# Kernel tuning notes

Hardware: AMD Instinct MI355X
Metric: run time of the kernel (lower is better)

Reference implementation:

```python
import jax, jax.numpy as jnp
import numpy as np
import math

B, N, F, H, T = 2, 1024, 8, 64, 16
E_R, E_C, EA = 8192, 32768, 4
NF = N * F


def _pos_enc(t_steps, h):
    pe = np.zeros((t_steps, h), dtype=np.float32)
    pos = np.arange(t_steps, dtype=np.float32)[:, None]
    div = np.exp(np.arange(0, h, 2, dtype=np.float32) * -(math.log(10000.0) / h))
    pe[:, 0::2] = np.sin(pos * div)
    pe[:, 1::2] = np.cos(pos * div)
    return jnp.asarray(pe)


def _ln(x, g, b, eps=1e-5):
    m = x.mean(-1, keepdims=True)
    v = jnp.var(x, axis=-1, keepdims=True)
    return (x - m) / jnp.sqrt(v + eps) * g + b


def _lrelu(x):
    return jnp.where(x >= 0, x, 0.01 * x)


def setup_inputs() -> dict:
    key = jax.random.key(0)
    ks = jax.random.split(key, 40)
    s = 0.05
    inp = {
        'x_global': jax.random.normal(ks[0], (B, N, H, T), jnp.float32),
        'per_feature_x': jax.random.normal(ks[1], (B, N, F, H, T), jnp.float32),
        'river_edge_attr': jax.random.uniform(ks[2], (E_R, EA), jnp.float32),
        'causal_edge_weight': jax.random.uniform(ks[3], (E_C,), jnp.float32),
        'W_tc': jax.random.normal(ks[4], (H, H, 3), jnp.float32) * s,
        'b_tc': jnp.zeros((H,), jnp.float32),
        'r_lin_W': jax.random.normal(ks[5], (H, H), jnp.float32) * s,
        'r_lin_b': jnp.zeros((H,), jnp.float32),
        'r_upd_W': jax.random.normal(ks[6], (2 * H, H), jnp.float32) * s,
        'r_upd_b': jnp.zeros((H,), jnp.float32),
        'r_edge_W': jax.random.normal(ks[7], (EA, 1), jnp.float32) * s,
        'r_edge_b': jnp.zeros((1,), jnp.float32),
        'r_gate': jnp.ones((1,), jnp.float32) * 0.3,
        'c_lin_W': jax.random.normal(ks[8], (H, H), jnp.float32) * s,
        'c_lin_b': jnp.zeros((H,), jnp.float32),
        'c_upd_W': jax.random.normal(ks[9], (2 * H, H), jnp.float32) * s,
        'c_upd_b': jnp.zeros((H,), jnp.float32),
        'c_gate': jnp.ones((1,), jnp.float32) * 0.3,
        'sf_W': jax.random.normal(ks[10], (2 * H, H), jnp.float32) * s,
        'sf_b': jnp.zeros((H,), jnp.float32),
        'femb': jax.random.normal(ks[11], (F, H), jnp.float32) * 0.02,
        'pfn_g': jnp.ones((H,), jnp.float32),
        'pfn_b': jnp.zeros((H,), jnp.float32),
        'f1_W': jax.random.normal(ks[12], (2 * H, H), jnp.float32) * s,
        'f1_b': jnp.zeros((H,), jnp.float32),
        'fln_g': jnp.ones((H,), jnp.float32),
        'fln_b': jnp.zeros((H,), jnp.float32),
        'f2_W': jax.random.normal(ks[13], (H, H), jnp.float32) * s,
        'f2_b': jnp.zeros((H,), jnp.float32),
        'river_edge_index': jax.random.randint(ks[14], (2, E_R), 0, N, jnp.int64),
        'causal_edge_index': jax.random.randint(ks[15], (2, E_C), 0, NF, jnp.int64),
    }
    return inp


def reference(x_global, per_feature_x, river_edge_attr, causal_edge_weight,
              W_tc, b_tc, r_lin_W, r_lin_b, r_upd_W, r_upd_b, r_edge_W, r_edge_b, r_gate,
              c_lin_W, c_lin_b, c_upd_W, c_upd_b, c_gate, sf_W, sf_b, femb,
              pfn_g, pfn_b, f1_W, f1_b, fln_g, fln_b, f2_W, f2_b,
              river_edge_index, causal_edge_index):
    b_, n_, h_, t_ = x_global.shape
    f_ = per_feature_x.shape[2]
    nf = n_ * f_

    # ---- river graph conv (vectorized over B,T) ----
    x_bt = jnp.transpose(x_global, (0, 3, 1, 2))  # [B,T,N,H]
    ew = (river_edge_attr @ r_edge_W + r_edge_b)[:, 0]  # edge_encoder -> [E_r]
    mw_r = jnp.clip(jax.nn.sigmoid(r_gate) * ew, 0.0, 1.0)
    src_r, tgt_r = river_edge_index[0], river_edge_index[1]
    lx = x_bt @ r_lin_W + r_lin_b
    msg_r = lx[:, :, src_r, :] * mw_r[None, None, :, None]  # [B,T,E_r,H]
    agg_r = jnp.zeros_like(x_bt).at[:, :, tgt_r, :].add(msg_r)
    river_upd = _lrelu(jnp.concatenate([agg_r, x_bt], -1) @ r_upd_W + r_upd_b)

    # ---- causal graph conv on (basin, feature) nodes ----
    pf_bt = jnp.transpose(per_feature_x, (0, 4, 1, 2, 3))  # [B,T,N,F,H]
    nodes = (pf_bt + femb[None, None, None]).reshape(b_, t_, nf, h_)
    mw_c = jnp.clip(jax.nn.sigmoid(c_gate) * causal_edge_weight, 0.0, 1.0)
    src_c, tgt_c = causal_edge_index[0], causal_edge_index[1]
    clx = nodes @ c_lin_W + c_lin_b
    msg_c = clx[:, :, src_c, :] * mw_c[None, None, :, None]  # [B,T,E_c,H]
    agg_c = jnp.zeros_like(nodes).at[:, :, tgt_c, :].add(msg_c)
    cupd = _lrelu(jnp.concatenate([agg_c, nodes], -1) @ c_upd_W + c_upd_b)
    cupd = cupd.reshape(b_, t_, n_, f_, h_)

    # per-feature layernorm over H, then to [B,N,F,H,T]
    pf_out = _ln(cupd, pfn_g, pfn_b)
    pf_out = jnp.transpose(pf_out, (0, 2, 3, 4, 1))

    causal_pooled = cupd.mean(axis=3)  # [B,T,N,H]
    x_spatial = jax.nn.silu(jnp.concatenate([river_upd, causal_pooled], -1) @ sf_W + sf_b)

    # ---- temporal conv with sin/cos positional encoding ----
    pe = _pos_enc(t_, h_)
    xt = jnp.transpose(x_global, (0, 1, 3, 2)) + pe[None, None]  # [B,N,T,H]
    x_nch = jnp.transpose(xt.reshape(b_ * n_, t_, h_), (0, 2, 1))  # [BN,H,T]
    y = jax.lax.conv_general_dilated(x_nch, W_tc, (1,), [(1, 1)],
                                     dimension_numbers=('NCH', 'OIH', 'NCH'))
    y = y + b_tc[None, :, None]
    x_temporal = jnp.transpose(y, (0, 2, 1)).reshape(b_, n_, t_, h_)

    # ---- fusion ----
    x_sp_bnth = jnp.transpose(x_spatial, (0, 2, 1, 3))  # [B,N,T,H]
    fz = jnp.concatenate([x_temporal, x_sp_bnth], -1) @ f1_W + f1_b
    fz = jax.nn.silu(_ln(fz, fln_g, fln_b))
    fz = fz @ f2_W + f2_b
    x_out = jnp.transpose(fz, (0, 1, 3, 2))  # [B,N,H,T]
    return (x_out, pf_out)
```

## Files before the change

kernel.cpp:

```cpp
#include <hip/hip_runtime.h>
#include <cstddef>

#define BB 2
#define NN 1024
#define FF 8
#define HH 64
#define TT 16
#define ER 8192
#define EC 32768
#define EA 4
#define NFD 8192
#define BTT 32
#define LDA 68

__device__ __forceinline__ void tile_gemm(const float* At, const float* Wt,
                                          float4 acc[4], int r0, int c0) {
#pragma unroll 16
  for (int k = 0; k < 64; ++k) {
    int rsw = r0 ^ (((k >> 4) & 3) << 2);
    float4 a = *(const float4*)(At + k * LDA + rsw);
    float4 b = *(const float4*)(Wt + k * LDA + c0);
    acc[0].x = fmaf(a.x, b.x, acc[0].x); acc[0].y = fmaf(a.x, b.y, acc[0].y);
    acc[0].z = fmaf(a.x, b.z, acc[0].z); acc[0].w = fmaf(a.x, b.w, acc[0].w);
    acc[1].x = fmaf(a.y, b.x, acc[1].x); acc[1].y = fmaf(a.y, b.y, acc[1].y);
    acc[1].z = fmaf(a.y, b.z, acc[1].z); acc[1].w = fmaf(a.y, b.w, acc[1].w);
    acc[2].x = fmaf(a.z, b.x, acc[2].x); acc[2].y = fmaf(a.z, b.y, acc[2].y);
    acc[2].z = fmaf(a.z, b.z, acc[2].z); acc[2].w = fmaf(a.z, b.w, acc[2].w);
    acc[3].x = fmaf(a.w, b.x, acc[3].x); acc[3].y = fmaf(a.w, b.y, acc[3].y);
    acc[3].z = fmaf(a.w, b.z, acc[3].z); acc[3].w = fmaf(a.w, b.w, acc[3].w);
  }
}

__device__ __forceinline__ void stage_W(float* Wt, const float* __restrict__ W, int tid) {
#pragma unroll
  for (int q = 0; q < 4; ++q) {
    int i = tid + q * 256;
    int k = i >> 4, c4 = (i & 15) << 2;
    *(float4*)(Wt + k * LDA + c4) = *(const float4*)(W + k * 64 + c4);
  }
}

__device__ __forceinline__ void stage_AT(float* At, const float* __restrict__ src, int tid) {
  int row = tid >> 2, kc = (tid & 3) << 4;
  int rsw = row ^ ((tid & 3) << 2);
  if (src) {
#pragma unroll
    for (int q = 0; q < 4; ++q) {
      float4 v = *(const float4*)(src + kc + q * 4);
      int k = kc + q * 4;
      At[(k + 0) * LDA + rsw] = v.x;
      At[(k + 1) * LDA + rsw] = v.y;
      At[(k + 2) * LDA + rsw] = v.z;
      At[(k + 3) * LDA + rsw] = v.w;
    }
  } else {
#pragma unroll
    for (int q = 0; q < 16; ++q) At[(kc + q) * LDA + rsw] = 0.f;
  }
}

#define FMA4(P, V) \
  P.x = fmaf(w, V.x, P.x); P.y = fmaf(w, V.y, P.y); \
  P.z = fmaf(w, V.z, P.z); P.w = fmaf(w, V.w, P.w);

__device__ __forceinline__ void stage_gather(float* At, float* s_sh,
                                             const float* __restrict__ slice, int rowbase,
                                             const int2* __restrict__ eg,
                                             const int* __restrict__ off, int tid) {
  int row = tid >> 2, kc = (tid & 3) << 4;
  int rsw = row ^ ((tid & 3) << 2);
  float4 p0 = make_float4(0.f, 0.f, 0.f, 0.f), p1 = p0, p2 = p0, p3 = p0;
  float s = 0.f;
  int node = rowbase + row;
  int e0 = off[node], e1 = off[node + 1];
  int j = e0;
  for (; j + 2 <= e1; j += 2) {
    int2 ea = eg[j], eb = eg[j + 1];
    float wa = __int_as_float(ea.y), wb = __int_as_float(eb.y);
    const float4* spa = (const float4*)(slice + (size_t)ea.x * 64 + kc);
    const float4* spb = (const float4*)(slice + (size_t)eb.x * 64 + kc);
    float4 a0 = spa[0], a1 = spa[1], a2 = spa[2], a3 = spa[3];
    float4 b0 = spb[0], b1 = spb[1], b2 = spb[2], b3 = spb[3];
    { float w = wa; FMA4(p0, a0); FMA4(p1, a1); FMA4(p2, a2); FMA4(p3, a3); }
    { float w = wb; FMA4(p0, b0); FMA4(p1, b1); FMA4(p2, b2); FMA4(p3, b3); }
    s += wa + wb;
  }
  if (j < e1) {
    int2 ea = eg[j];
    float w = __int_as_float(ea.y);
    const float4* spa = (const float4*)(slice + (size_t)ea.x * 64 + kc);
    float4 a0 = spa[0], a1 = spa[1], a2 = spa[2], a3 = spa[3];
    FMA4(p0, a0); FMA4(p1, a1); FMA4(p2, a2); FMA4(p3, a3);
    s += w;
  }
  At[(kc + 0) * LDA + rsw] = p0.x;  At[(kc + 1) * LDA + rsw] = p0.y;
  At[(kc + 2) * LDA + rsw] = p0.z;  At[(kc + 3) * LDA + rsw] = p0.w;
  At[(kc + 4) * LDA + rsw] = p1.x;  At[(kc + 5) * LDA + rsw] = p1.y;
  At[(kc + 6) * LDA + rsw] = p1.z;  At[(kc + 7) * LDA + rsw] = p1.w;
  At[(kc + 8) * LDA + rsw] = p2.x;  At[(kc + 9) * LDA + rsw] = p2.y;
  At[(kc + 10) * LDA + rsw] = p2.z; At[(kc + 11) * LDA + rsw] = p2.w;
  At[(kc + 12) * LDA + rsw] = p3.x; At[(kc + 13) * LDA + rsw] = p3.y;
  At[(kc + 14) * LDA + rsw] = p3.z; At[(kc + 15) * LDA + rsw] = p3.w;
  if ((tid & 3) == 0) s_sh[row] = s;
}

template <bool POOL>
__global__ __launch_bounds__(256, 4) void k_gnn(const float* __restrict__ base,
    const int* __restrict__ off, const int2* __restrict__ eg,
    const float* __restrict__ Wf, const float* __restrict__ Wbot,
    const float* __restrict__ vv, const float* __restrict__ bb,
    float* __restrict__ out, float* __restrict__ pooled,
    int ngShift, int rowsSlice) {
  __shared__ float At[64 * LDA];
  __shared__ float Wt[64 * LDA];
  __shared__ float s_sh[64];
  int tid = threadIdx.x;
  int bid = blockIdx.x;
  int xcd = bid & 7;
  int slot = bid >> 3;
  int ng = slot & ((1 << ngShift) - 1);
  int bt = xcd + 8 * (slot >> ngShift);
  const float* slice = base + (size_t)bt * rowsSlice * 64;
  int rowbase = ng * 64;
  float4 z4 = make_float4(0.f, 0.f, 0.f, 0.f);
  float4 acc[4] = {z4, z4, z4, z4};
  int r0 = (tid >> 4) << 2, c0 = (tid & 15) << 2;

  stage_W(Wt, Wf, tid);
  stage_gather(At, s_sh, slice, rowbase, eg, off, tid);
  __syncthreads();
  tile_gemm(At, Wt, acc, r0, c0);
  __syncthreads();

  stage_W(Wt, Wbot, tid);
  stage_AT(At, slice + (size_t)(rowbase + (tid >> 2)) * 64, tid);
  __syncthreads();
  tile_gemm(At, Wt, acc, r0, c0);

  float4 v4 = *(const float4*)(vv + c0);
  float4 b4 = *(const float4*)(bb + c0);
  float4 zz[4];
#pragma unroll
  for (int i = 0; i < 4; ++i) {
    int row = r0 + i;
    float sv = s_sh[row];
    float4 z;
    z.x = acc[i].x + sv * v4.x + b4.x;
    z.y = acc[i].y + sv * v4.y + b4.y;
    z.z = acc[i].z + sv * v4.z + b4.z;
    z.w = acc[i].w + sv * v4.w + b4.w;
    z.x = z.x >= 0.f ? z.x : 0.01f * z.x;
    z.y = z.y >= 0.f ? z.y : 0.01f * z.y;
    z.z = z.z >= 0.f ? z.z : 0.01f * z.z;
    z.w = z.w >= 0.f ? z.w : 0.01f * z.w;
    zz[i] = z;
    *(float4*)(out + ((size_t)bt * rowsSlice + rowbase + row) * 64 + c0) = z;
  }

  if (POOL) {
    float4 ps;
    ps.x = zz[0].x + zz[1].x + zz[2].x + zz[3].x;
    ps.y = zz[0].y + zz[1].y + zz[2].y + zz[3].y;
    ps.z = zz[0].z + zz[1].z + zz[2].z + zz[3].z;
    ps.w = zz[0].w + zz[1].w + zz[2].w + zz[3].w;
    ps.x += __shfl_xor(ps.x, 16);
    ps.y += __shfl_xor(ps.y, 16);
    ps.z += __shfl_xor(ps.z, 16);
    ps.w += __shfl_xor(ps.w, 16);
    if (((tid >> 4) & 1) == 0) {
      int nd = r0 >> 3;
      float4 o;
      o.x = ps.x * 0.125f; o.y = ps.y * 0.125f;
      o.z = ps.z * 0.125f; o.w = ps.w * 0.125f;
      *(float4*)(pooled + ((size_t)bt * NN + (rowbase >> 3) + nd) * 64 + c0) = o;
    }
  }
}

__global__ __launch_bounds__(256, 4) void k_sf2(const float* __restrict__ river_upd,
    const float* __restrict__ pooled, const float* __restrict__ sf_W,
    const float* __restrict__ sf_b, float* __restrict__ x_spatial) {
  __shared__ float At[64 * LDA];
  __shared__ float Wt[64 * LDA];
  int tid = threadIdx.x;
  int rowbase = blockIdx.x * 64;
  float4 z4 = make_float4(0.f, 0.f, 0.f, 0.f);
  float4 acc[4] = {z4, z4, z4, z4};
  int r0 = (tid >> 4) << 2, c0 = (tid & 15) << 2;

  stage_W(Wt, sf_W, tid);
  stage_AT(At, river_upd + (size_t)(rowbase + (tid >> 2)) * 64, tid);
  __syncthreads();
  tile_gemm(At, Wt, acc, r0, c0);
  __syncthreads();

  stage_W(Wt, sf_W + 4096, tid);
  stage_AT(At, pooled + (size_t)(rowbase + (tid >> 2)) * 64, tid);
  __syncthreads();
  tile_gemm(At, Wt, acc, r0, c0);

  float4 b4 = *(const float4*)(sf_b + c0);
#pragma unroll
  for (int i = 0; i < 4; ++i) {
    float4 z;
    z.x = acc[i].x + b4.x; z.y = acc[i].y + b4.y;
    z.z = acc[i].z + b4.z; z.w = acc[i].w + b4.w;
    z.x = z.x / (1.f + expf(-z.x)); z.y = z.y / (1.f + expf(-z.y));
    z.z = z.z / (1.f + expf(-z.z)); z.w = z.w / (1.f + expf(-z.w));
    *(float4*)(x_spatial + (size_t)(rowbase + r0 + i) * 64 + c0) = z;
  }
}

__global__ __launch_bounds__(256, 4) void k_fuse2(const float* __restrict__ xt,
    const float* __restrict__ xsp, const float* __restrict__ Wg,
    const float* __restrict__ cvec, const float* __restrict__ f1W,
    const float* __restrict__ flng, const float* __restrict__ flnb,
    const float* __restrict__ f2W, const float* __restrict__ f2b,
    float* __restrict__ x_out) {
  __shared__ float At[64 * LDA];
  __shared__ float Wt[64 * LDA];
  int tid = threadIdx.x;
  int bn0 = blockIdx.x * 4;
  int srow = tid >> 2;
  int bnl = srow >> 4, t = srow & 15;
  int bn = bn0 + bnl;
  float4 z4 = make_float4(0.f, 0.f, 0.f, 0.f);
  float4 acc[4] = {z4, z4, z4, z4};
  int r0 = (tid >> 4) << 2, c0 = (tid & 15) << 2;

#pragma unroll
  for (int kt = 0; kt < 3; ++kt) {
    int t2 = t + kt - 1;
    const float* src = (t2 >= 0 && t2 < TT) ? xt + ((size_t)bn * TT + t2) * 64 : nullptr;
    stage_W(Wt, Wg + kt * 4096, tid);
    stage_AT(At, src, tid);
    __syncthreads();
    tile_gemm(At, Wt, acc, r0, c0);
    __syncthreads();
  }
  {
    int b = bn >> 10, n = bn & 1023;
    const float* src = xsp + ((size_t)(b * TT + t) * NN + n) * 64;
    stage_W(Wt, f1W + 4096, tid);
    stage_AT(At, src, tid);
    __syncthreads();
    tile_gemm(At, Wt, acc, r0, c0);
    __syncthreads();
  }

  float4 cv = *(const float4*)(cvec + c0);
  float4 g4 = *(const float4*)(flng + c0);
  float4 lb4 = *(const float4*)(flnb + c0);
  float4 zz[4];
#pragma unroll
  for (int i = 0; i < 4; ++i) {
    zz[i].x = acc[i].x + cv.x; zz[i].y = acc[i].y + cv.y;
    zz[i].z = acc[i].z + cv.z; zz[i].w = acc[i].w + cv.w;
    float ps = zz[i].x + zz[i].y + zz[i].z + zz[i].w;
    float pq = zz[i].x * zz[i].x + zz[i].y * zz[i].y + zz[i].z * zz[i].z + zz[i].w * zz[i].w;
    ps += __shfl_xor(ps, 1); pq += __shfl_xor(pq, 1);
    ps += __shfl_xor(ps, 2); pq += __shfl_xor(pq, 2);
    ps += __shfl_xor(ps, 4); pq += __shfl_xor(pq, 4);
    ps += __shfl_xor(ps, 8); pq += __shfl_xor(pq, 8);
    float m = ps * (1.f / 64.f);
    float var = pq * (1.f / 64.f) - m * m;
    float inv = rsqrtf(var + 1e-5f);
    float4 w;
    w.x = (zz[i].x - m) * inv * g4.x + lb4.x;
    w.y = (zz[i].y - m) * inv * g4.y + lb4.y;
    w.z = (zz[i].z - m) * inv * g4.z + lb4.z;
    w.w = (zz[i].w - m) * inv * g4.w + lb4.w;
    zz[i].x = w.x / (1.f + expf(-w.x));
    zz[i].y = w.y / (1.f + expf(-w.y));
    zz[i].z = w.z / (1.f + expf(-w.z));
    zz[i].w = w.w / (1.f + expf(-w.w));
  }
  {
    int xsw = ((c0 >> 4) & 3) << 2;
#pragma unroll
    for (int i = 0; i < 4; ++i) {
      int rr = (r0 + i) ^ xsw;
      At[(c0 + 0) * LDA + rr] = zz[i].x;
      At[(c0 + 1) * LDA + rr] = zz[i].y;
      At[(c0 + 2) * LDA + rr] = zz[i].z;
      At[(c0 + 3) * LDA + rr] = zz[i].w;
    }
  }
  stage_W(Wt, f2W, tid);
  __syncthreads();
  float4 acc2[4] = {z4, z4, z4, z4};
  tile_gemm(At, Wt, acc2, r0, c0);
  __syncthreads();
  float4 f2b4 = *(const float4*)(f2b + c0);
#pragma unroll
  for (int i = 0; i < 4; ++i) {
    float4 o;
    o.x = acc2[i].x + f2b4.x; o.y = acc2[i].y + f2b4.y;
    o.z = acc2[i].z + f2b4.z; o.w = acc2[i].w + f2b4.w;
    *(float4*)(Wt + (r0 + i) * LDA + c0) = o;
  }
  __syncthreads();
#pragma unroll
  for (int q = 0; q < 4; ++q) {
    int idx = tid + q * 256;
    int fo = idx * 4;
    int bnl2 = fo >> 10, rem = fo & 1023;
    int c = rem >> 4, tt = rem & 15;
    float4 o;
    o.x = Wt[(bnl2 * 16 + tt + 0) * LDA + c];
    o.y = Wt[(bnl2 * 16 + tt + 1) * LDA + c];
    o.z = Wt[(bnl2 * 16 + tt + 2) * LDA + c];
    o.w = Wt[(bnl2 * 16 + tt + 3) * LDA + c];
    *(float4*)(x_out + (size_t)(bn0 + bnl2) * 1024 + rem) = o;
  }
}

__global__ void k_prep_edges(const float* __restrict__ attr, const float* __restrict__ cw,
                             const float* __restrict__ reW, const float* __restrict__ reB,
                             const float* __restrict__ rgate, const float* __restrict__ cgate,
                             float* __restrict__ mw_r, float* __restrict__ mw_c,
                             int* __restrict__ rcnt, int* __restrict__ ccnt) {
  int i = blockIdx.x * 256 + threadIdx.x;
  if (i < EC) {
    float g = 1.f / (1.f + expf(-cgate[0]));
    mw_c[i] = fminf(fmaxf(g * cw[i], 0.f), 1.f);
  }
  if (i < ER) {
    float ew = reB[0];
#pragma unroll
    for (int a = 0; a < EA; ++a) ew += attr[i * EA + a] * reW[a];
    float g = 1.f / (1.f + expf(-rgate[0]));
    mw_r[i] = fminf(fmaxf(g * ew, 0.f), 1.f);
  }
  if (i < NN) rcnt[i] = 0;
  if (i < NFD) ccnt[i] = 0;
}

__global__ void k_prep_w(const float* __restrict__ r_lin_W, const float* __restrict__ r_upd_W,
                         const float* __restrict__ r_lin_b,
                         const float* __restrict__ c_lin_W, const float* __restrict__ c_upd_W,
                         const float* __restrict__ c_lin_b,
                         const float* __restrict__ W_tc, const float* __restrict__ b_tc,
                         const float* __restrict__ f1_W, const float* __restrict__ f1_b,
                         float* __restrict__ Wfr, float* __restrict__ v_r,
                         float* __restrict__ Wfc, float* __restrict__ v_c,
                         float* __restrict__ Wg, float* __restrict__ cvec) {
  int tid = threadIdx.x;
  if (blockIdx.x == 0) {
    for (int idx = tid; idx < 4096; idx += 256) {
      int k = idx >> 6, j = idx & 63;
      float s = 0.f;
      for (int m = 0; m < 64; ++m) s += r_lin_W[k * 64 + m] * r_upd_W[m * 64 + j];
      Wfr[idx] = s;
    }
    if (tid < 64) {
      float s = 0.f;
      for (int m = 0; m < 64; ++m) s += r_lin_b[m] * r_upd_W[m * 64 + tid];
      v_r[tid] = s;
    }
  } else if (blockIdx.x == 1) {
    for (int idx = tid; idx < 4096; idx += 256) {
      int k = idx >> 6, j = idx & 63;
      float s = 0.f;
      for (int m = 0; m < 64; ++m) s += c_lin_W[k * 64 + m] * c_upd_W[m * 64 + j];
      Wfc[idx] = s;
    }
    if (tid < 64) {
      float s = 0.f;
      for (int m = 0; m < 64; ++m) s += c_lin_b[m] * c_upd_W[m * 64 + tid];
      v_c[tid] = s;
    }
  } else {
    for (int idx = tid; idx < 12288; idx += 256) {
      int r = idx >> 6, c = idx & 63;
      int kk = r >> 6, i = r & 63;
      float s = 0.f;
      for (int o = 0; o < 64; ++o) s += W_tc[o * 192 + i * 3 + kk] * f1_W[o * 64 + c];
      Wg[idx] = s;
    }
    if (tid < 64) {
      float s = f1_b[tid];
      for (int o = 0; o < 64; ++o) s += b_tc[o] * f1_W[o * 64 + tid];
      cvec[tid] = s;
    }
  }
}

__global__ void k_count(const int* __restrict__ ridx, const int* __restrict__ cidx,
                        int* __restrict__ rcnt, int* __restrict__ ccnt) {
  int e = blockIdx.x * 256 + threadIdx.x;
  if (e < ER) atomicAdd(&rcnt[ridx[ER + e]], 1);
  if (e < EC) atomicAdd(&ccnt[cidx[EC + e]], 1);
}

template <int ITEMS>
__device__ __forceinline__ void scan_impl(const int* __restrict__ cnt, int n,
                                          int* __restrict__ off, int* __restrict__ cur,
                                          int* sh) {
  int tid = threadIdx.x;
  int local[ITEMS];
  int s = 0;
  int base = tid * ITEMS;
#pragma unroll
  for (int j = 0; j < ITEMS; ++j) { local[j] = cnt[base + j]; s += local[j]; }
  sh[tid] = s;
  __syncthreads();
  for (int d = 1; d < 1024; d <<= 1) {
    int v = (tid >= d) ? sh[tid - d] : 0;
    __syncthreads();
    sh[tid] += v;
    __syncthreads();
  }
  int excl = tid ? sh[tid - 1] : 0;
#pragma unroll
  for (int j = 0; j < ITEMS; ++j) { off[base + j] = excl; cur[base + j] = excl; excl += local[j]; }
  if (tid == 1023) off[n] = excl;
}

__global__ __launch_bounds__(1024) void k_scan(const int* __restrict__ rcnt, int* __restrict__ roff,
                                               int* __restrict__ rcur,
                                               const int* __restrict__ ccnt, int* __restrict__ coff,
                                               int* __restrict__ ccur) {
  __shared__ int sh[1024];
  if (blockIdx.x == 0) scan_impl<1>(rcnt, NN, roff, rcur, sh);
  else                 scan_impl<8>(ccnt, NFD, coff, ccur, sh);
}

__global__ void k_fill(const int* __restrict__ ridx, const int* __restrict__ cidx,
                       const float* __restrict__ mw_r, const float* __restrict__ mw_c,
                       int* __restrict__ rcur, int* __restrict__ ccur,
                       int2* __restrict__ rpk, int2* __restrict__ cpk) {
  int e = blockIdx.x * 256 + threadIdx.x;
  if (e < ER) {
    int t = ridx[ER + e]; int p = atomicAdd(&rcur[t], 1);
    rpk[p] = make_int2(ridx[e], __float_as_int(mw_r[e]));
  }
  if (e < EC) {
    int t = cidx[EC + e]; int p = atomicAdd(&ccur[t], 1);
    cpk[p] = make_int2(cidx[e], __float_as_int(mw_c[e]));
  }
}

__global__ void k_xpose(const float* __restrict__ xg, float* __restrict__ x_bt,
                        float* __restrict__ xt) {
  __shared__ float lds[64][17];
  int bn = blockIdx.x;
  int b = bn >> 10, n = bn & 1023;
  int tid = threadIdx.x;
  const float* src = xg + (size_t)bn * (HH * TT);
  for (int i = tid; i < 1024; i += 256) lds[i >> 4][i & 15] = src[i];
  __syncthreads();
  for (int i = tid; i < 1024; i += 256) {
    int t = i >> 6, h = i & 63;
    float v = lds[h][t];
    float div = expf(-(float)(h & ~1) * (9.210340371976184f / 64.f));
    float arg = (float)t * div;
    float pe = (h & 1) ? cosf(arg) : sinf(arg);
    xt[(size_t)bn * 1024 + i] = v + pe;
    x_bt[(((size_t)b * TT + t) * NN + n) * HH + h] = v;
  }
}

__global__ void k_nodes(const float* __restrict__ pfx, const float* __restrict__ femb,
                        float* __restrict__ nodes) {
  __shared__ float lds[64][17];
  int bnf = blockIdx.x;
  int f = bnf & 7;
  int n = (bnf >> 3) & 1023;
  int b = bnf >> 13;
  int tid = threadIdx.x;
  const float* src = pfx + (size_t)bnf * (HH * TT);
  for (int i = tid; i < 1024; i += 256) lds[i >> 4][i & 15] = src[i];
  __syncthreads();
  for (int i = tid; i < 1024; i += 256) {
    int t = i >> 6, h = i & 63;
    nodes[(((size_t)b * TT + t) * NFD + n * FF + f) * HH + h] = lds[h][t] + femb[f * HH + h];
  }
}

__global__ void k_pfout(const float* __restrict__ cupd, const float* __restrict__ g,
                        const float* __restrict__ be, float* __restrict__ pf_out) {
  __shared__ float lds[16][65];
  __shared__ float mi[16], rs[16];
  int bnf = blockIdx.x;
  int f = bnf & 7;
  int n = (bnf >> 3) & 1023;
  int b = bnf >> 13;
  int tid = threadIdx.x;
  for (int i = tid; i < 1024; i += 256) {
    int t = i >> 6, h = i & 63;
    lds[t][h] = cupd[(((size_t)b * TT + t) * NFD + n * FF + f) * HH + h];
  }
  __syncthreads();
  int t = tid >> 4, l = tid & 15;
  float sm = 0.f;
#pragma unroll
  for (int q = 0; q < 4; ++q) sm += lds[t][l + 16 * q];
  sm += __shfl_xor(sm, 1); sm += __shfl_xor(sm, 2); sm += __shfl_xor(sm, 4); sm += __shfl_xor(sm, 8);
  float m = sm * (1.f / 64.f);
  float sv = 0.f;
#pragma unroll
  for (int q = 0; q < 4; ++q) { float d = lds[t][l + 16 * q] - m; sv += d * d; }
  sv += __shfl_xor(sv, 1); sv += __shfl_xor(sv, 2); sv += __shfl_xor(sv, 4); sv += __shfl_xor(sv, 8);
  float inv = 1.f / sqrtf(sv * (1.f / 64.f) + 1e-5f);
  if (l == 0) { mi[t] = m; rs[t] = inv; }
  __syncthreads();
  float* out = pf_out + (size_t)bnf * (HH * TT);
  for (int i = tid; i < 1024; i += 256) {
    int h = i >> 4, tt = i & 15;
    out[i] = (lds[tt][h] - mi[tt]) * rs[tt] * g[h] + be[h];
  }
}

extern "C" void kernel_launch(void* const* d_in, const int* in_sizes, int n_in,
                              void* d_out, int out_size, void* d_ws, size_t ws_size,
                              hipStream_t stream) {
  (void)in_sizes; (void)n_in; (void)out_size; (void)ws_size;
  const float* x_global     = (const float*)d_in[0];
  const float* per_feature  = (const float*)d_in[1];
  const float* r_edge_attr  = (const float*)d_in[2];
  const float* c_edge_w     = (const float*)d_in[3];
  const float* W_tc         = (const float*)d_in[4];
  const float* b_tc         = (const float*)d_in[5];
  const float* r_lin_W      = (const float*)d_in[6];
  const float* r_lin_b      = (const float*)d_in[7];
  const float* r_upd_W      = (const float*)d_in[8];
  const float* r_upd_b      = (const float*)d_in[9];
  const float* r_edge_W     = (const float*)d_in[10];
  const float* r_edge_b     = (const float*)d_in[11];
  const float* r_gate       = (const float*)d_in[12];
  const float* c_lin_W      = (const float*)d_in[13];
  const float* c_lin_b      = (const float*)d_in[14];
  const float* c_upd_W      = (const float*)d_in[15];
  const float* c_upd_b      = (const float*)d_in[16];
  const float* c_gate       = (const float*)d_in[17];
  const float* sf_W         = (const float*)d_in[18];
  const float* sf_b         = (const float*)d_in[19];
  const float* femb         = (const float*)d_in[20];
  const float* pfn_g        = (const float*)d_in[21];
  const float* pfn_b        = (const float*)d_in[22];
  const float* f1_W         = (const float*)d_in[23];
  const float* f1_b         = (const float*)d_in[24];
  const float* fln_g        = (const float*)d_in[25];
  const float* fln_b        = (const float*)d_in[26];
  const float* f2_W         = (const float*)d_in[27];
  const float* f2_b         = (const float*)d_in[28];
  const int*   ridx         = (const int*)d_in[29];
  const int*   cidx         = (const int*)d_in[30];

  float* out_f = (float*)d_out;
  float* x_out  = out_f;
  float* pf_out = out_f + 2097152;

  const size_t BTNFH = (size_t)BTT * NFD * HH;
  const size_t BTNH  = (size_t)BTT * NN * HH;

  float* ws = (float*)d_ws;
  size_t o = 0;
  float* nodes      = ws + o; o += BTNFH;
  float* cupd       = ws + o; o += BTNFH;
  float* x_bt       = ws + o; o += BTNH;
  float* xt         = ws + o; o += BTNH;
  float* river_upd  = ws + o; o += BTNH;
  float* pooled     = ws + o; o += BTNH;
  float* x_spatial  = ws + o; o += BTNH;
  float* mw_r       = ws + o; o += ER;
  float* mw_c       = ws + o; o += EC;
  float* Wfr        = ws + o; o += 4096;
  float* v_r        = ws + o; o += 64;
  float* Wfc        = ws + o; o += 4096;
  float* v_c        = ws + o; o += 64;
  float* Wg         = ws + o; o += 192 * 64;
  float* cvec       = ws + o; o += 64;
  int2* rpk = (int2*)(ws + o);
  int2* cpk = rpk + ER;
  int* ib = (int*)(cpk + EC);
  size_t io = 0;
  int* rcnt    = ib + io; io += NN;
  int* roff    = ib + io; io += NN + 1;
  int* rcur    = ib + io; io += NN + 1;
  int* ccnt    = ib + io; io += NFD;
  int* coff    = ib + io; io += NFD + 1;
  int* ccur    = ib + io; io += NFD + 1;

  k_prep_edges<<<128, 256, 0, stream>>>(r_edge_attr, c_edge_w, r_edge_W, r_edge_b,
                                        r_gate, c_gate, mw_r, mw_c, rcnt, ccnt);
  k_prep_w<<<3, 256, 0, stream>>>(r_lin_W, r_upd_W, r_lin_b, c_lin_W, c_upd_W, c_lin_b,
                                  W_tc, b_tc, f1_W, f1_b, Wfr, v_r, Wfc, v_c, Wg, cvec);
  k_count<<<128, 256, 0, stream>>>(ridx, cidx, rcnt, ccnt);
  k_scan<<<2, 1024, 0, stream>>>(rcnt, roff, rcur, ccnt, coff, ccur);
  k_fill<<<128, 256, 0, stream>>>(ridx, cidx, mw_r, mw_c, rcur, ccur, rpk, cpk);
  k_xpose<<<BB * NN, 256, 0, stream>>>(x_global, x_bt, xt);
  k_nodes<<<BB * NN * FF, 256, 0, stream>>>(per_feature, femb, nodes);
  k_gnn<false><<<BTT * 16, 256, 0, stream>>>(x_bt, roff, rpk,
                                             Wfr, r_upd_W + 4096, v_r, r_upd_b,
                                             river_upd, nullptr, 4, NN);
  k_gnn<true><<<BTT * 128, 256, 0, stream>>>(nodes, coff, cpk,
                                             Wfc, c_upd_W + 4096, v_c, c_upd_b,
                                             cupd, pooled, 7, NFD);
  k_pfout<<<BB * NN * FF, 256, 0, stream>>>(cupd, pfn_g, pfn_b, pf_out);
  k_sf2<<<512, 256, 0, stream>>>(river_upd, pooled, sf_W, sf_b, x_spatial);
  k_fuse2<<<512, 256, 0, stream>>>(xt, x_spatial, Wg, cvec, f1_W, fln_g, fln_b,
                                   f2_W, f2_b, x_out);
}
```

Measured before the change: 482.1 us.

## Merge independent kernels into combined launches and retile the edge gather

```diff
diff --git a/kernel.cpp b/kernel.cpp
--- a/kernel.cpp
+++ b/kernel.cpp
@@ -59,75 +59,93 @@
   }
 }
 
-#define FMA4(P, V) \
-  P.x = fmaf(w, V.x, P.x); P.y = fmaf(w, V.y, P.y); \
-  P.z = fmaf(w, V.z, P.z); P.w = fmaf(w, V.w, P.w);
-
-__device__ __forceinline__ void stage_gather(float* At, float* s_sh,
-                                             const float* __restrict__ slice, int rowbase,
-                                             const int2* __restrict__ eg,
-                                             const int* __restrict__ off, int tid) {
-  int row = tid >> 2, kc = (tid & 3) << 4;
-  int rsw = row ^ ((tid & 3) << 2);
-  float4 p0 = make_float4(0.f, 0.f, 0.f, 0.f), p1 = p0, p2 = p0, p3 = p0;
-  float s = 0.f;
-  int node = rowbase + row;
-  int e0 = off[node], e1 = off[node + 1];
-  int j = e0;
-  for (; j + 2 <= e1; j += 2) {
-    int2 ea = eg[j], eb = eg[j + 1];
-    float wa = __int_as_float(ea.y), wb = __int_as_float(eb.y);
-    const float4* spa = (const float4*)(slice + (size_t)ea.x * 64 + kc);
-    const float4* spb = (const float4*)(slice + (size_t)eb.x * 64 + kc);
-    float4 a0 = spa[0], a1 = spa[1], a2 = spa[2], a3 = spa[3];
-    float4 b0 = spb[0], b1 = spb[1], b2 = spb[2], b3 = spb[3];
-    { float w = wa; FMA4(p0, a0); FMA4(p1, a1); FMA4(p2, a2); FMA4(p3, a3); }
-    { float w = wb; FMA4(p0, b0); FMA4(p1, b1); FMA4(p2, b2); FMA4(p3, b3); }
-    s += wa + wb;
-  }
-  if (j < e1) {
-    int2 ea = eg[j];
-    float w = __int_as_float(ea.y);
-    const float4* spa = (const float4*)(slice + (size_t)ea.x * 64 + kc);
-    float4 a0 = spa[0], a1 = spa[1], a2 = spa[2], a3 = spa[3];
-    FMA4(p0, a0); FMA4(p1, a1); FMA4(p2, a2); FMA4(p3, a3);
-    s += w;
-  }
-  At[(kc + 0) * LDA + rsw] = p0.x;  At[(kc + 1) * LDA + rsw] = p0.y;
-  At[(kc + 2) * LDA + rsw] = p0.z;  At[(kc + 3) * LDA + rsw] = p0.w;
-  At[(kc + 4) * LDA + rsw] = p1.x;  At[(kc + 5) * LDA + rsw] = p1.y;
-  At[(kc + 6) * LDA + rsw] = p1.z;  At[(kc + 7) * LDA + rsw] = p1.w;
-  At[(kc + 8) * LDA + rsw] = p2.x;  At[(kc + 9) * LDA + rsw] = p2.y;
-  At[(kc + 10) * LDA + rsw] = p2.z; At[(kc + 11) * LDA + rsw] = p2.w;
-  At[(kc + 12) * LDA + rsw] = p3.x; At[(kc + 13) * LDA + rsw] = p3.y;
-  At[(kc + 14) * LDA + rsw] = p3.z; At[(kc + 15) * LDA + rsw] = p3.w;
-  if ((tid & 3) == 0) s_sh[row] = s;
-}
-
-template <bool POOL>
-__global__ __launch_bounds__(256, 4) void k_gnn(const float* __restrict__ base,
-    const int* __restrict__ off, const int2* __restrict__ eg,
-    const float* __restrict__ Wf, const float* __restrict__ Wbot,
-    const float* __restrict__ vv, const float* __restrict__ bb,
-    float* __restrict__ out, float* __restrict__ pooled,
-    int ngShift, int rowsSlice) {
+#define GFMA(ACC, W, V) \
+  ACC.x = fmaf(W, V.x, ACC.x); ACC.y = fmaf(W, V.y, ACC.y); \
+  ACC.z = fmaf(W, V.z, ACC.z); ACC.w = fmaf(W, V.w, ACC.w);
+
+__device__ __forceinline__ void stage_gather16(float* At, float* s_sh,
+                                               const float* __restrict__ slice, int rowbase,
+                                               const int2* __restrict__ eg,
+                                               const int* __restrict__ off, int tid) {
+  int rloc = tid >> 4;
+  int lane = tid & 15;
+  int kc = lane << 2;
+  int xsw = (lane >> 2) << 2;
+#pragma unroll
+  for (int p = 0; p < 4; ++p) {
+    int row = p * 16 + rloc;
+    int node = rowbase + row;
+    int e0 = off[node], e1 = off[node + 1];
+    float4 acc = make_float4(0.f, 0.f, 0.f, 0.f);
+    float s = 0.f;
+    int j = e0;
+    for (; j + 4 <= e1; j += 4) {
+      int2 e_0 = eg[j], e_1 = eg[j + 1], e_2 = eg[j + 2], e_3 = eg[j + 3];
+      float w0 = __int_as_float(e_0.y), w1 = __int_as_float(e_1.y);
+      float w2 = __int_as_float(e_2.y), w3 = __int_as_float(e_3.y);
+      float4 v0 = *(const float4*)(slice + (size_t)e_0.x * 64 + kc);
+      float4 v1 = *(const float4*)(slice + (size_t)e_1.x * 64 + kc);
+      float4 v2 = *(const float4*)(slice + (size_t)e_2.x * 64 + kc);
+      float4 v3 = *(const float4*)(slice + (size_t)e_3.x * 64 + kc);
+      GFMA(acc, w0, v0); GFMA(acc, w1, v1); GFMA(acc, w2, v2); GFMA(acc, w3, v3);
+      s += w0 + w1 + w2 + w3;
+    }
+    for (; j < e1; ++j) {
+      int2 e_0 = eg[j];
+      float w0 = __int_as_float(e_0.y);
+      float4 v0 = *(const float4*)(slice + (size_t)e_0.x * 64 + kc);
+      GFMA(acc, w0, v0);
+      s += w0;
+    }
+    int rsw = row ^ xsw;
+    At[(kc + 0) * LDA + rsw] = acc.x;
+    At[(kc + 1) * LDA + rsw] = acc.y;
+    At[(kc + 2) * LDA + rsw] = acc.z;
+    At[(kc + 3) * LDA + rsw] = acc.w;
+    if (lane == 0) s_sh[row] = s;
+  }
+}
+
+__global__ __launch_bounds__(256, 4) void k_gnn(
+    const float* __restrict__ xbt, const float* __restrict__ nodes,
+    const int* __restrict__ roff, const int2* __restrict__ rpk,
+    const int* __restrict__ coff, const int2* __restrict__ cpk,
+    const float* __restrict__ Wfr, const float* __restrict__ rWbot,
+    const float* __restrict__ v_r, const float* __restrict__ r_b,
+    const float* __restrict__ Wfc, const float* __restrict__ cWbot,
+    const float* __restrict__ v_c, const float* __restrict__ c_b,
+    float* __restrict__ river_out, float* __restrict__ cupd,
+    float* __restrict__ pooled) {
   __shared__ float At[64 * LDA];
   __shared__ float Wt[64 * LDA];
   __shared__ float s_sh[64];
   int tid = threadIdx.x;
   int bid = blockIdx.x;
-  int xcd = bid & 7;
-  int slot = bid >> 3;
-  int ng = slot & ((1 << ngShift) - 1);
-  int bt = xcd + 8 * (slot >> ngShift);
+  const float *base, *Wf, *Wbot, *vv, *bb;
+  const int* off; const int2* eg;
+  float* out; float* pool;
+  int rowsSlice, rowbase, bt;
+  if (bid < 512) {
+    int xcd = bid & 7, slot = bid >> 3;
+    rowsSlice = NN; rowbase = (slot & 15) * 64; bt = xcd + 8 * (slot >> 4);
+    base = xbt; off = roff; eg = rpk;
+    Wf = Wfr; Wbot = rWbot; vv = v_r; bb = r_b;
+    out = river_out; pool = nullptr;
+  } else {
+    int cb = bid - 512;
+    int xcd = cb & 7, slot = cb >> 3;
+    rowsSlice = NFD; rowbase = (slot & 127) * 64; bt = xcd + 8 * (slot >> 7);
+    base = nodes; off = coff; eg = cpk;
+    Wf = Wfc; Wbot = cWbot; vv = v_c; bb = c_b;
+    out = cupd; pool = pooled;
+  }
   const float* slice = base + (size_t)bt * rowsSlice * 64;
-  int rowbase = ng * 64;
   float4 z4 = make_float4(0.f, 0.f, 0.f, 0.f);
   float4 acc[4] = {z4, z4, z4, z4};
   int r0 = (tid >> 4) << 2, c0 = (tid & 15) << 2;
 
   stage_W(Wt, Wf, tid);
-  stage_gather(At, s_sh, slice, rowbase, eg, off, tid);
+  stage_gather16(At, s_sh, slice, rowbase, eg, off, tid);
   __syncthreads();
   tile_gemm(At, Wt, acc, r0, c0);
   __syncthreads();
@@ -157,7 +175,7 @@
     *(float4*)(out + ((size_t)bt * rowsSlice + rowbase + row) * 64 + c0) = z;
   }
 
-  if (POOL) {
+  if (pool) {
     float4 ps;
     ps.x = zz[0].x + zz[1].x + zz[2].x + zz[3].x;
     ps.y = zz[0].y + zz[1].y + zz[2].y + zz[3].y;
@@ -177,37 +195,73 @@
   }
 }
 
-__global__ __launch_bounds__(256, 4) void k_sf2(const float* __restrict__ river_upd,
-    const float* __restrict__ pooled, const float* __restrict__ sf_W,
-    const float* __restrict__ sf_b, float* __restrict__ x_spatial) {
+__global__ __launch_bounds__(256, 4) void k_post(
+    const float* __restrict__ river_upd, const float* __restrict__ pooled,
+    const float* __restrict__ sf_W, const float* __restrict__ sf_b,
+    float* __restrict__ x_spatial,
+    const float* __restrict__ cupd, const float* __restrict__ g,
+    const float* __restrict__ be, float* __restrict__ pf_out) {
   __shared__ float At[64 * LDA];
   __shared__ float Wt[64 * LDA];
   int tid = threadIdx.x;
-  int rowbase = blockIdx.x * 64;
-  float4 z4 = make_float4(0.f, 0.f, 0.f, 0.f);
-  float4 acc[4] = {z4, z4, z4, z4};
-  int r0 = (tid >> 4) << 2, c0 = (tid & 15) << 2;
-
-  stage_W(Wt, sf_W, tid);
-  stage_AT(At, river_upd + (size_t)(rowbase + (tid >> 2)) * 64, tid);
-  __syncthreads();
-  tile_gemm(At, Wt, acc, r0, c0);
-  __syncthreads();
-
-  stage_W(Wt, sf_W + 4096, tid);
-  stage_AT(At, pooled + (size_t)(rowbase + (tid >> 2)) * 64, tid);
-  __syncthreads();
-  tile_gemm(At, Wt, acc, r0, c0);
-
-  float4 b4 = *(const float4*)(sf_b + c0);
-#pragma unroll
-  for (int i = 0; i < 4; ++i) {
-    float4 z;
-    z.x = acc[i].x + b4.x; z.y = acc[i].y + b4.y;
-    z.z = acc[i].z + b4.z; z.w = acc[i].w + b4.w;
-    z.x = z.x / (1.f + expf(-z.x)); z.y = z.y / (1.f + expf(-z.y));
-    z.z = z.z / (1.f + expf(-z.z)); z.w = z.w / (1.f + expf(-z.w));
-    *(float4*)(x_spatial + (size_t)(rowbase + r0 + i) * 64 + c0) = z;
+  int bid = blockIdx.x;
+  if (bid < 512) {
+    int rowbase = bid * 64;
+    float4 z4 = make_float4(0.f, 0.f, 0.f, 0.f);
+    float4 acc[4] = {z4, z4, z4, z4};
+    int r0 = (tid >> 4) << 2, c0 = (tid & 15) << 2;
+
+    stage_W(Wt, sf_W, tid);
+    stage_AT(At, river_upd + (size_t)(rowbase + (tid >> 2)) * 64, tid);
+    __syncthreads();
+    tile_gemm(At, Wt, acc, r0, c0);
+    __syncthreads();
+
+    stage_W(Wt, sf_W + 4096, tid);
+    stage_AT(At, pooled + (size_t)(rowbase + (tid >> 2)) * 64, tid);
+    __syncthreads();
+    tile_gemm(At, Wt, acc, r0, c0);
+
+    float4 b4 = *(const float4*)(sf_b + c0);
+#pragma unroll
+    for (int i = 0; i < 4; ++i) {
+      float4 z;
+      z.x = acc[i].x + b4.x; z.y = acc[i].y + b4.y;
+      z.z = acc[i].z + b4.z; z.w = acc[i].w + b4.w;
+      z.x = z.x / (1.f + expf(-z.x)); z.y = z.y / (1.f + expf(-z.y));
+      z.z = z.z / (1.f + expf(-z.z)); z.w = z.w / (1.f + expf(-z.w));
+      *(float4*)(x_spatial + (size_t)(rowbase + r0 + i) * 64 + c0) = z;
+    }
+  } else {
+    float* l16 = At;
+    float* mi = Wt; float* rs = Wt + 16;
+    int bnf = bid - 512;
+    int f = bnf & 7;
+    int n = (bnf >> 3) & 1023;
+    int b = bnf >> 13;
+    for (int i = tid; i < 1024; i += 256) {
+      int t = i >> 6, h = i & 63;
+      l16[t * 65 + h] = cupd[(((size_t)b * TT + t) * NFD + n * FF + f) * HH + h];
+    }
+    __syncthreads();
+    int t = tid >> 4, l = tid & 15;
+    float sm = 0.f;
+#pragma unroll
+    for (int q = 0; q < 4; ++q) sm += l16[t * 65 + l + 16 * q];
+    sm += __shfl_xor(sm, 1); sm += __shfl_xor(sm, 2); sm += __shfl_xor(sm, 4); sm += __shfl_xor(sm, 8);
+    float m = sm * (1.f / 64.f);
+    float sv = 0.f;
+#pragma unroll
+    for (int q = 0; q < 4; ++q) { float d = l16[t * 65 + l + 16 * q] - m; sv += d * d; }
+    sv += __shfl_xor(sv, 1); sv += __shfl_xor(sv, 2); sv += __shfl_xor(sv, 4); sv += __shfl_xor(sv, 8);
+    float inv = 1.f / sqrtf(sv * (1.f / 64.f) + 1e-5f);
+    if (l == 0) { mi[t] = m; rs[t] = inv; }
+    __syncthreads();
+    float* out = pf_out + (size_t)bnf * (HH * TT);
+    for (int i = tid; i < 1024; i += 256) {
+      int h = i >> 4, tt = i & 15;
+      out[i] = (l16[tt * 65 + h] - mi[tt]) * rs[tt] * g[h] + be[h];
+    }
   }
 }
 
@@ -315,73 +369,56 @@
   }
 }
 
-__global__ void k_prep_edges(const float* __restrict__ attr, const float* __restrict__ cw,
-                             const float* __restrict__ reW, const float* __restrict__ reB,
-                             const float* __restrict__ rgate, const float* __restrict__ cgate,
-                             float* __restrict__ mw_r, float* __restrict__ mw_c,
-                             int* __restrict__ rcnt, int* __restrict__ ccnt) {
-  int i = blockIdx.x * 256 + threadIdx.x;
-  if (i < EC) {
-    float g = 1.f / (1.f + expf(-cgate[0]));
-    mw_c[i] = fminf(fmaxf(g * cw[i], 0.f), 1.f);
-  }
-  if (i < ER) {
-    float ew = reB[0];
-#pragma unroll
-    for (int a = 0; a < EA; ++a) ew += attr[i * EA + a] * reW[a];
-    float g = 1.f / (1.f + expf(-rgate[0]));
-    mw_r[i] = fminf(fmaxf(g * ew, 0.f), 1.f);
-  }
-  if (i < NN) rcnt[i] = 0;
-  if (i < NFD) ccnt[i] = 0;
-}
-
-__global__ void k_prep_w(const float* __restrict__ r_lin_W, const float* __restrict__ r_upd_W,
-                         const float* __restrict__ r_lin_b,
-                         const float* __restrict__ c_lin_W, const float* __restrict__ c_upd_W,
-                         const float* __restrict__ c_lin_b,
-                         const float* __restrict__ W_tc, const float* __restrict__ b_tc,
-                         const float* __restrict__ f1_W, const float* __restrict__ f1_b,
-                         float* __restrict__ Wfr, float* __restrict__ v_r,
-                         float* __restrict__ Wfc, float* __restrict__ v_c,
-                         float* __restrict__ Wg, float* __restrict__ cvec) {
+__global__ void k_prep(const float* __restrict__ attr, const float* __restrict__ cw,
+                       const float* __restrict__ reW, const float* __restrict__ reB,
+                       const float* __restrict__ rgate, const float* __restrict__ cgate,
+                       float* __restrict__ mw_r, float* __restrict__ mw_c,
+                       int* __restrict__ rcnt, int* __restrict__ ccnt,
+                       const float* __restrict__ r_lin_W, const float* __restrict__ r_upd_W,
+                       const float* __restrict__ r_lin_b,
+                       const float* __restrict__ c_lin_W, const float* __restrict__ c_upd_W,
+                       const float* __restrict__ c_lin_b,
+                       const float* __restrict__ W_tc, const float* __restrict__ b_tc,
+                       const float* __restrict__ f1_W, const float* __restrict__ f1_b,
+                       float* __restrict__ Wfr, float* __restrict__ v_r,
+                       float* __restrict__ Wfc, float* __restrict__ v_c,
+                       float* __restrict__ Wg, float* __restrict__ cvec) {
+  int bid = blockIdx.x;
   int tid = threadIdx.x;
-  if (blockIdx.x == 0) {
-    for (int idx = tid; idx < 4096; idx += 256) {
-      int k = idx >> 6, j = idx & 63;
-      float s = 0.f;
-      for (int m = 0; m < 64; ++m) s += r_lin_W[k * 64 + m] * r_upd_W[m * 64 + j];
-      Wfr[idx] = s;
-    }
-    if (tid < 64) {
-      float s = 0.f;
-      for (int m = 0; m < 64; ++m) s += r_lin_b[m] * r_upd_W[m * 64 + tid];
-      v_r[tid] = s;
-    }
-  } else if (blockIdx.x == 1) {
-    for (int idx = tid; idx < 4096; idx += 256) {
-      int k = idx >> 6, j = idx & 63;
-      float s = 0.f;
-      for (int m = 0; m < 64; ++m) s += c_lin_W[k * 64 + m] * c_upd_W[m * 64 + j];
-      Wfc[idx] = s;
-    }
-    if (tid < 64) {
-      float s = 0.f;
-      for (int m = 0; m < 64; ++m) s += c_lin_b[m] * c_upd_W[m * 64 + tid];
-      v_c[tid] = s;
-    }
+  if (bid < 128) {
+    int i = bid * 256 + tid;
+    if (i < EC) {
+      float gg = 1.f / (1.f + expf(-cgate[0]));
+      mw_c[i] = fminf(fmaxf(gg * cw[i], 0.f), 1.f);
+    }
+    if (i < ER) {
+      float ew = reB[0];
+#pragma unroll
+      for (int a = 0; a < EA; ++a) ew += attr[i * EA + a] * reW[a];
+      float gg = 1.f / (1.f + expf(-rgate[0]));
+      mw_r[i] = fminf(fmaxf(gg * ew, 0.f), 1.f);
+    }
+    if (i < NN) rcnt[i] = 0;
+    if (i < NFD) ccnt[i] = 0;
   } else {
-    for (int idx = tid; idx < 12288; idx += 256) {
-      int r = idx >> 6, c = idx & 63;
-      int kk = r >> 6, i = r & 63;
-      float s = 0.f;
-      for (int o = 0; o < 64; ++o) s += W_tc[o * 192 + i * 3 + kk] * f1_W[o * 64 + c];
-      Wg[idx] = s;
-    }
-    if (tid < 64) {
-      float s = f1_b[tid];
-      for (int o = 0; o < 64; ++o) s += b_tc[o] * f1_W[o * 64 + tid];
-      cvec[tid] = s;
+    int r = (bid - 128) * 4 + (tid >> 6);
+    int j = tid & 63;
+    const float* abase = nullptr;
+    const float* bmat = nullptr;
+    float* dst = nullptr;
+    int astride = 1;
+    if (r < 64)        { abase = r_lin_W + r * 64; bmat = r_upd_W; dst = Wfr + r * 64; }
+    else if (r < 128)  { int rr = r - 64; abase = c_lin_W + rr * 64; bmat = c_upd_W; dst = Wfc + rr * 64; }
+    else if (r < 320)  { int rr = r - 128; int kk = rr >> 6, i2 = rr & 63;
+                         abase = W_tc + i2 * 3 + kk; astride = 192; bmat = f1_W; dst = Wg + rr * 64; }
+    else if (r == 320) { abase = r_lin_b; bmat = r_upd_W; dst = v_r; }
+    else if (r == 321) { abase = c_lin_b; bmat = c_upd_W; dst = v_c; }
+    else if (r == 322) { abase = b_tc; bmat = f1_W; dst = cvec; }
+    if (dst) {
+      float s = (r == 322) ? f1_b[j] : 0.f;
+#pragma unroll 8
+      for (int m = 0; m < 64; ++m) s += abase[m * astride] * bmat[m * 64 + j];
+      dst[j] = s;
     }
   }
 }
@@ -441,74 +478,40 @@
   }
 }
 
-__global__ void k_xpose(const float* __restrict__ xg, float* __restrict__ x_bt,
-                        float* __restrict__ xt) {
-  __shared__ float lds[64][17];
-  int bn = blockIdx.x;
-  int b = bn >> 10, n = bn & 1023;
-  int tid = threadIdx.x;
-  const float* src = xg + (size_t)bn * (HH * TT);
-  for (int i = tid; i < 1024; i += 256) lds[i >> 4][i & 15] = src[i];
-  __syncthreads();
-  for (int i = tid; i < 1024; i += 256) {
-    int t = i >> 6, h = i & 63;
-    float v = lds[h][t];
-    float div = expf(-(float)(h & ~1) * (9.210340371976184f / 64.f));
-    float arg = (float)t * div;
-    float pe = (h & 1) ? cosf(arg) : sinf(arg);
-    xt[(size_t)bn * 1024 + i] = v + pe;
-    x_bt[(((size_t)b * TT + t) * NN + n) * HH + h] = v;
-  }
-}
-
-__global__ void k_nodes(const float* __restrict__ pfx, const float* __restrict__ femb,
+__global__ void k_trans(const float* __restrict__ xg, float* __restrict__ x_bt,
+                        float* __restrict__ xt,
+                        const float* __restrict__ pfx, const float* __restrict__ femb,
                         float* __restrict__ nodes) {
   __shared__ float lds[64][17];
-  int bnf = blockIdx.x;
-  int f = bnf & 7;
-  int n = (bnf >> 3) & 1023;
-  int b = bnf >> 13;
+  int bid = blockIdx.x;
   int tid = threadIdx.x;
-  const float* src = pfx + (size_t)bnf * (HH * TT);
-  for (int i = tid; i < 1024; i += 256) lds[i >> 4][i & 15] = src[i];
-  __syncthreads();
-  for (int i = tid; i < 1024; i += 256) {
-    int t = i >> 6, h = i & 63;
-    nodes[(((size_t)b * TT + t) * NFD + n * FF + f) * HH + h] = lds[h][t] + femb[f * HH + h];
-  }
-}
-
-__global__ void k_pfout(const float* __restrict__ cupd, const float* __restrict__ g,
-                        const float* __restrict__ be, float* __restrict__ pf_out) {
-  __shared__ float lds[16][65];
-  __shared__ float mi[16], rs[16];
-  int bnf = blockIdx.x;
-  int f = bnf & 7;
-  int n = (bnf >> 3) & 1023;
-  int b = bnf >> 13;
-  int tid = threadIdx.x;
-  for (int i = tid; i < 1024; i += 256) {
-    int t = i >> 6, h = i & 63;
-    lds[t][h] = cupd[(((size_t)b * TT + t) * NFD + n * FF + f) * HH + h];
-  }
-  __syncthreads();
-  int t = tid >> 4, l = tid & 15;
-  float sm = 0.f;
-#pragma unroll
-  for (int q = 0; q < 4; ++q) sm += lds[t][l + 16 * q];
-  sm += __shfl_xor(sm, 1); sm += __shfl_xor(sm, 2); sm += __shfl_xor(sm, 4); sm += __shfl_xor(sm, 8);
-  float m = sm * (1.f / 64.f);
-  float sv = 0.f;
-#pragma unroll
-  for (int q = 0; q < 4; ++q) { float d = lds[t][l + 16 * q] - m; sv += d * d; }
-  sv += __shfl_xor(sv, 1); sv += __shfl_xor(sv, 2); sv += __shfl_xor(sv, 4); sv += __shfl_xor(sv, 8);
-  float inv = 1.f / sqrtf(sv * (1.f / 64.f) + 1e-5f);
-  if (l == 0) { mi[t] = m; rs[t] = inv; }
-  __syncthreads();
-  float* out = pf_out + (size_t)bnf * (HH * TT);
-  for (int i = tid; i < 1024; i += 256) {
-    int h = i >> 4, tt = i & 15;
-    out[i] = (lds[tt][h] - mi[tt]) * rs[tt] * g[h] + be[h];
+  if (bid < 2048) {
+    int bn = bid;
+    int b = bn >> 10, n = bn & 1023;
+    const float* src = xg + (size_t)bn * (HH * TT);
+    for (int i = tid; i < 1024; i += 256) lds[i >> 4][i & 15] = src[i];
+    __syncthreads();
+    for (int i = tid; i < 1024; i += 256) {
+      int t = i >> 6, h = i & 63;
+      float v = lds[h][t];
+      float div = expf(-(float)(h & ~1) * (9.210340371976184f / 64.f));
+      float arg = (float)t * div;
+      float pe = (h & 1) ? cosf(arg) : sinf(arg);
+      xt[(size_t)bn * 1024 + i] = v + pe;
+      x_bt[(((size_t)b * TT + t) * NN + n) * HH + h] = v;
+    }
+  } else {
+    int bnf = bid - 2048;
+    int f = bnf & 7;
+    int n = (bnf >> 3) & 1023;
+    int b = bnf >> 13;
+    const float* src = pfx + (size_t)bnf * (HH * TT);
+    for (int i = tid; i < 1024; i += 256) lds[i >> 4][i & 15] = src[i];
+    __syncthreads();
+    for (int i = tid; i < 1024; i += 256) {
+      int t = i >> 6, h = i & 63;
+      nodes[(((size_t)b * TT + t) * NFD + n * FF + f) * HH + h] = lds[h][t] + femb[f * HH + h];
+    }
   }
 }
 
@@ -583,23 +586,22 @@
   int* coff    = ib + io; io += NFD + 1;
   int* ccur    = ib + io; io += NFD + 1;
 
-  k_prep_edges<<<128, 256, 0, stream>>>(r_edge_attr, c_edge_w, r_edge_W, r_edge_b,
-                                        r_gate, c_gate, mw_r, mw_c, rcnt, ccnt);
-  k_prep_w<<<3, 256, 0, stream>>>(r_lin_W, r_upd_W, r_lin_b, c_lin_W, c_upd_W, c_lin_b,
-                                  W_tc, b_tc, f1_W, f1_b, Wfr, v_r, Wfc, v_c, Wg, cvec);
+  k_prep<<<209, 256, 0, stream>>>(r_edge_attr, c_edge_w, r_edge_W, r_edge_b,
+                                  r_gate, c_gate, mw_r, mw_c, rcnt, ccnt,
+                                  r_lin_W, r_upd_W, r_lin_b, c_lin_W, c_upd_W, c_lin_b,
+                                  W_tc, b_tc, f1_W, f1_b,
+                                  Wfr, v_r, Wfc, v_c, Wg, cvec);
   k_count<<<128, 256, 0, stream>>>(ridx, cidx, rcnt, ccnt);
   k_scan<<<2, 1024, 0, stream>>>(rcnt, roff, rcur, ccnt, coff, ccur);
   k_fill<<<128, 256, 0, stream>>>(ridx, cidx, mw_r, mw_c, rcur, ccur, rpk, cpk);
-  k_xpose<<<BB * NN, 256, 0, stream>>>(x_global, x_bt, xt);
-  k_nodes<<<BB * NN * FF, 256, 0, stream>>>(per_feature, femb, nodes);
-  k_gnn<false><<<BTT * 16, 256, 0, stream>>>(x_bt, roff, rpk,
+  k_trans<<<2048 + BB * NN * FF, 256, 0, stream>>>(x_global, x_bt, xt,
+                                                   per_feature, femb, nodes);
+  k_gnn<<<512 + BTT * 128, 256, 0, stream>>>(x_bt, nodes, roff, rpk, coff, cpk,
                                              Wfr, r_upd_W + 4096, v_r, r_upd_b,
-                                             river_upd, nullptr, 4, NN);
-  k_gnn<true><<<BTT * 128, 256, 0, stream>>>(nodes, coff, cpk,
                                              Wfc, c_upd_W + 4096, v_c, c_upd_b,
-                                             cupd, pooled, 7, NFD);
-  k_pfout<<<BB * NN * FF, 256, 0, stream>>>(cupd, pfn_g, pfn_b, pf_out);
-  k_sf2<<<512, 256, 0, stream>>>(river_upd, pooled, sf_W, sf_b, x_spatial);
+                                             river_upd, cupd, pooled);
+  k_post<<<512 + BB * NN * FF, 256, 0, stream>>>(river_upd, pooled, sf_W, sf_b,
+                                                 x_spatial, cupd, pfn_g, pfn_b, pf_out);
   k_fuse2<<<512, 256, 0, stream>>>(xt, x_spatial, Wg, cvec, f1_W, fln_g, fln_b,
                                    f2_W, f2_b, x_out);
 }
```

New measurement: 421.6 us. -12.5%, faster.
